# Kernel tuning notes

Measured on AMD Instinct MI355X. Metric: run time of the kernel, lower is better.

The kernel has to match this reference:

```python
import jax, jax.numpy as jnp
import numpy as np

D = 512      # d_x
H = 8        # n_I
DH = 64      # d_q = d_k = d_v = d_r
L = 4        # n_L
NUM_KNOTS = 5
ORDER = 3
KNOTS = np.linspace(-1.0, 1.0, NUM_KNOTS + ORDER)  # 8 uniform knots
EPS = 1e-5


def layernorm(x, w, b):
    mu = jnp.mean(x, axis=-1, keepdims=True)
    var = jnp.mean((x - mu) ** 2, axis=-1, keepdims=True)
    return (x - mu) * jax.lax.rsqrt(var + EPS) * w + b


def bspline_basis(x):
    # Cox-de Boor recursion on uniform knots, vectorized over all knot indices.
    # x: [...]; returns [..., len(KNOTS)-1-ORDER] = [..., 4]
    t = KNOTS
    B = jnp.stack([((t[k] <= x) & (x < t[k + 1])).astype(x.dtype)
                   for k in range(len(t) - 1)], axis=-1)
    for m in range(1, ORDER + 1):
        cols = []
        for k in range(len(t) - 1 - m):
            left = (x - t[k]) / (t[k + m] - t[k]) * B[..., k]
            right = (t[k + m + 1] - x) / (t[k + m + 1] - t[k + 1]) * B[..., k + 1]
            cols.append(left + right)
        B = jnp.stack(cols, axis=-1)
    return B


def setup_inputs() -> dict:
    key = jax.random.key(0)
    ks = jax.random.split(key, 20)
    B_, S = 4, 1024
    inp = {
        "src": jax.random.normal(ks[0], (B_, S, D), dtype=jnp.float32),
        "ln1_w": jnp.ones((L, D)), "ln1_b": jnp.zeros((L, D)),
        "ln2_w": jnp.ones((L, D)), "ln2_b": jnp.zeros((L, D)),
        "ln3_w": jnp.ones((L, D)), "ln3_b": jnp.zeros((L, D)),
        "Wq_w": jax.random.normal(ks[1], (L, H * DH, D)) * 0.02,
        "Wq_b": jnp.zeros((L, H * DH)),
        "Wk_w": jax.random.normal(ks[2], (L, H * DH, D)) * 0.02,
        "Wk_b": jnp.zeros((L, H * DH)),
        "Wv_w": jax.random.normal(ks[3], (L, H * DH, D)) * 0.02,
        "Wv_b": jnp.zeros((L, H * DH)),
        "Wr_w": jax.random.normal(ks[4], (L, H * DH, D)) * (1.0 / np.sqrt(DH)),
        "Wr_b": jnp.zeros((L, H * DH)),
        "Wo_w": jax.random.normal(ks[5], (L, D, H * DH)) * 0.02,
        "Wo_b": jnp.zeros((L, D)),
        "inner_c": jax.random.normal(ks[6], (L, D, NUM_KNOTS)) * 0.1,
        "outer_c": jax.random.normal(ks[7], (L, D, D)) * 0.1,
        "src_mask": jnp.ones((B_, 1, 1, S), dtype=jnp.int32),
    }
    return inp


def reference(src, ln1_w, ln1_b, ln2_w, ln2_b, ln3_w, ln3_b,
              Wq_w, Wq_b, Wk_w, Wk_b, Wv_w, Wv_b, Wr_w, Wr_b, Wo_w, Wo_b,
              inner_c, outer_c, src_mask):
    bsz, S, _ = src.shape
    scale = 1.0 / np.sqrt(DH)
    for l in range(L):
        # --- self-attention block ---
        z = layernorm(src, ln1_w[l], ln1_b[l])
        def heads(W, b):
            return (z @ W.T + b).reshape(bsz, S, H, DH).transpose(0, 2, 1, 3)
        Q = heads(Wq_w[l], Wq_b[l])
        K = heads(Wk_w[l], Wk_b[l])
        V = heads(Wv_w[l], Wv_b[l])
        R = heads(Wr_w[l], Wr_b[l])
        dot = jnp.einsum('bhid,bhjd->bhij', Q, K) * scale
        dot = jnp.where(src_mask == 0, -1e10, dot)
        att = jax.nn.softmax(dot, axis=-1)
        v_bar = jnp.einsum('bhjd,bhij->bhid', V, att)
        new_v = (v_bar * R).transpose(0, 2, 1, 3).reshape(bsz, S, H * DH)
        src = src + new_v @ Wo_w[l].T + Wo_b[l]
        # --- KAN feedforward block ---
        z = layernorm(src, ln2_w[l], ln2_b[l])
        xt = jnp.tanh(z)
        basis = bspline_basis(xt)            # [b,s,D,4]
        nb = NUM_KNOTS - ORDER               # only first 2 basis fns used
        inner = jnp.einsum('bsdk,dk->bsd', basis[..., :nb], inner_c[l][:, :nb])
        out = jnp.einsum('bsd,od->bso', inner, outer_c[l])
        src = src + out
        src = layernorm(src, ln3_w[l], ln3_b[l])
    return src
```

## Files before the change

### kernel.cpp

```cpp
#include <hip/hip_runtime.h>

#define B_   4
#define S_   1024
#define D_   512
#define H_   8
#define DH_  64
#define L_   4
#define NTOK (B_ * S_)
#define NT   (NTOK * D_)
#define DD   (D_ * D_)

typedef __attribute__((ext_vector_type(8))) short bf16x8;
typedef __attribute__((ext_vector_type(4))) float f32x4;

#define GLL(gp, lp)                                                            \
    __builtin_amdgcn_global_load_lds(                                          \
        (const __attribute__((address_space(1))) unsigned int*)(gp),           \
        (__attribute__((address_space(3))) unsigned int*)(lp), 16, 0, 0)

__device__ __forceinline__ float us2f(unsigned short u) {
    unsigned int v = ((unsigned int)u) << 16;
    return __uint_as_float(v);
}
__device__ __forceinline__ unsigned short f2us(float f) {
    unsigned int u = __float_as_uint(f);
    unsigned int r = (u + 0x7fffu + ((u >> 16) & 1u)) >> 16;
    return (unsigned short)r;
}
__device__ __forceinline__ unsigned short f2us_trunc(float f) {
    return (unsigned short)(__float_as_uint(f) >> 16);
}

__device__ __forceinline__ float kan_inner(float zv, const float* __restrict__ ic, int n) {
    const float kn[8] = {-1.f,
                         -0.71428571428571430f, -0.42857142857142855f, -0.14285714285714285f,
                          0.14285714285714285f,  0.42857142857142855f,  0.71428571428571430f,
                          1.f};
    float xt = tanhf(zv);
    float B0[5];
#pragma unroll
    for (int k = 0; k < 5; ++k) B0[k] = (kn[k] <= xt && xt < kn[k + 1]) ? 1.f : 0.f;
    float B1[4];
#pragma unroll
    for (int k = 0; k < 4; ++k)
        B1[k] = (xt - kn[k]) / (kn[k + 1] - kn[k]) * B0[k] +
                (kn[k + 2] - xt) / (kn[k + 2] - kn[k + 1]) * B0[k + 1];
    float B2[3];
#pragma unroll
    for (int k = 0; k < 3; ++k)
        B2[k] = (xt - kn[k]) / (kn[k + 2] - kn[k]) * B1[k] +
                (kn[k + 3] - xt) / (kn[k + 3] - kn[k + 1]) * B1[k + 1];
    float B3[2];
#pragma unroll
    for (int k = 0; k < 2; ++k)
        B3[k] = (xt - kn[k]) / (kn[k + 3] - kn[k]) * B2[k] +
                (kn[k + 4] - xt) / (kn[k + 4] - kn[k + 1]) * B2[k + 1];
    return B3[0] * ic[n * 5 + 0] + B3[1] * ic[n * 5 + 1];
}

struct PreArgs {
    const float* w[6];
    unsigned short* cw;
    const float* src;
    const float* ln1w;
    const float* ln1b;
    float* srcf;
    unsigned short* z;
};
__global__ __launch_bounds__(256) void pre_k(PreArgs a) {
    int bx = blockIdx.x;
    if (bx < 6144) {
        int y = bx >> 8;
        int l = y / 6, tp = y - l * 6;
        int i = ((bx & 255) * 256 + threadIdx.x) * 4;
        float4 v = *(const float4*)(a.w[tp] + (size_t)l * DD + i);
        ushort4 o;
        o.x = f2us(v.x); o.y = f2us(v.y); o.z = f2us(v.z); o.w = f2us(v.w);
        *(ushort4*)(a.cw + (size_t)y * DD + i) = o;
    } else {
        int wv = threadIdx.x >> 6, lane = threadIdx.x & 63;
        int tok = (bx - 6144) * 4 + wv;
        const float* xr = a.src + (size_t)tok * D_;
        float v[8];
        float s = 0.f, s2 = 0.f;
#pragma unroll
        for (int i = 0; i < 8; ++i) {
            float t = xr[lane + 64 * i];
            v[i] = t; s += t; s2 += t * t;
        }
#pragma unroll
        for (int o = 1; o < 64; o <<= 1) { s += __shfl_xor(s, o); s2 += __shfl_xor(s2, o); }
        float mu = s * (1.f / D_);
        float var = s2 * (1.f / D_) - mu * mu;
        float rs = rsqrtf(var + 1e-5f);
#pragma unroll
        for (int i = 0; i < 8; ++i) {
            int d = lane + 64 * i;
            a.srcf[(size_t)tok * D_ + d] = v[i];
            a.z[(size_t)tok * D_ + d] = f2us((v[i] - mu) * rs * a.ln1w[d] + a.ln1b[d]);
        }
    }
}

struct MGemm128Args {
    const unsigned short* A;
    const unsigned short* W[4];
    const float* bias[4];
    unsigned short* C[4];
    int tflag[4];
};

__global__ __launch_bounds__(256) void mgemm128_k(MGemm128Args g) {
    __shared__ unsigned short As[2][128 * 64];
    __shared__ unsigned short Bs[2][128 * 64];
    int z = blockIdx.z;
    const unsigned short* W = g.W[z];
    const float* bias = g.bias[z];
    unsigned short* C = g.C[z];
    int m0 = blockIdx.y * 128, n0 = blockIdx.x * 128;
    int t = threadIdx.x;
    int wave = t >> 6, lane = t & 63;
    int wm = (wave >> 1) * 64, wn = (wave & 1) * 64;
    int l15 = lane & 15, quad = lane >> 4;
    int srow = lane >> 3, schunk = lane & 7;

    f32x4 acc[4][4];
#pragma unroll
    for (int i = 0; i < 4; ++i)
#pragma unroll
        for (int j = 0; j < 4; ++j)
#pragma unroll
            for (int r = 0; r < 4; ++r) acc[i][j][r] = 0.f;

    int rb = wave * 32;
    int swz = l15 & 7;

    #define STAGE128(buf, k0)                                                       \
        do {                                                                        \
            _Pragma("unroll")                                                       \
            for (int g8 = 0; g8 < 4; ++g8) {                                        \
                int row0 = rb + g8 * 8;                                             \
                int row = row0 + srow;                                              \
                int cg = schunk ^ (row & 7);                                        \
                GLL(g.A + (size_t)(m0 + row) * D_ + (k0) + cg * 8, &As[buf][row0 * 64]); \
                GLL(W   + (size_t)(n0 + row) * D_ + (k0) + cg * 8, &Bs[buf][row0 * 64]); \
            }                                                                       \
        } while (0)

    STAGE128(0, 0);

    int cur = 0;
    for (int ks = 0; ks < 8; ++ks) {
        if (ks < 7) {
            STAGE128(cur ^ 1, (ks + 1) * 64);
            asm volatile("s_waitcnt vmcnt(8)" ::: "memory");
        } else {
            asm volatile("s_waitcnt vmcnt(0)" ::: "memory");
        }
        __builtin_amdgcn_s_barrier();
        __builtin_amdgcn_sched_barrier(0);
#pragma unroll
        for (int kc = 0; kc < 2; ++kc) {
            int ch = ((kc * 4 + quad) ^ swz) * 8;
            bf16x8 af[4], bfr[4];
#pragma unroll
            for (int mt = 0; mt < 4; ++mt)
                af[mt] = *(const bf16x8*)&As[cur][(wm + mt * 16 + l15) * 64 + ch];
#pragma unroll
            for (int nt = 0; nt < 4; ++nt)
                bfr[nt] = *(const bf16x8*)&Bs[cur][(wn + nt * 16 + l15) * 64 + ch];
#pragma unroll
            for (int mt = 0; mt < 4; ++mt)
#pragma unroll
                for (int nt = 0; nt < 4; ++nt)
                    acc[mt][nt] = __builtin_amdgcn_mfma_f32_16x16x32_bf16(
                        af[mt], bfr[nt], acc[mt][nt], 0, 0, 0);
        }
        __builtin_amdgcn_sched_barrier(0);
        __builtin_amdgcn_s_barrier();
        cur ^= 1;
    }
    #undef STAGE128

    if (g.tflag[z]) {
#pragma unroll
        for (int mt = 0; mt < 4; ++mt)
#pragma unroll
            for (int nt = 0; nt < 4; ++nt) {
                int n = n0 + wn + nt * 16 + l15;
                float bv = bias[n];
                int m = m0 + wm + mt * 16 + quad * 4;
                ushort4 pk;
                pk.x = f2us(acc[mt][nt][0] + bv);
                pk.y = f2us(acc[mt][nt][1] + bv);
                pk.z = f2us(acc[mt][nt][2] + bv);
                pk.w = f2us(acc[mt][nt][3] + bv);
                *(ushort4*)(C + ((size_t)(m >> 10) * 512 + n) * 1024 + (m & 1023)) = pk;
            }
    } else {
#pragma unroll
        for (int mt = 0; mt < 4; ++mt)
#pragma unroll
            for (int nt = 0; nt < 4; ++nt) {
                int n = n0 + wn + nt * 16 + l15;
                float bv = bias[n];
#pragma unroll
                for (int r = 0; r < 4; ++r) {
                    int m = m0 + wm + mt * 16 + quad * 4 + r;
                    C[(size_t)m * D_ + n] = f2us(acc[mt][nt][r] + bv);
                }
            }
    }
}

template <int MODE>
__global__ __launch_bounds__(512) void gemmrow_k(
    const unsigned short* __restrict__ A, const unsigned short* __restrict__ W,
    const float* __restrict__ bias, const float* __restrict__ res,
    float* __restrict__ yf, unsigned short* __restrict__ zbo,
    const float* __restrict__ wA, const float* __restrict__ bA,
    const float* __restrict__ wB, const float* __restrict__ bB,
    const float* __restrict__ ic) {
    __shared__ unsigned short Bs[2][512 * 64];
    __shared__ unsigned short As[16 * 512];
    __shared__ float redS[16][8];
    __shared__ float redS2[16][8];

    int m0 = blockIdx.x * 16;
    int t = threadIdx.x, wave = t >> 6, lane = t & 63;
    int l15 = lane & 15, quad = lane >> 4;
    int srow = lane >> 3, schunk = lane & 7;
    int swz = l15 & 7;

#pragma unroll
    for (int rr = 0; rr < 2; ++rr) {
        int r = wave * 2 + rr;
        GLL(A + (size_t)(m0 + r) * D_ + (lane ^ (r & 7)) * 8, &As[r * 512]);
    }
    const unsigned short* Wp = W + (size_t)(wave * 64 + srow) * D_ + (schunk ^ srow) * 8;
#pragma unroll
    for (int g8 = 0; g8 < 8; ++g8)
        GLL(Wp + (size_t)g8 * 8 * D_, &Bs[0][(wave * 64 + g8 * 8) * 64]);
    asm volatile("s_waitcnt vmcnt(8)" ::: "memory");
    __builtin_amdgcn_s_barrier();

    f32x4 acc[4];
#pragma unroll
    for (int nt = 0; nt < 4; ++nt)
#pragma unroll
        for (int r = 0; r < 4; ++r) acc[nt][r] = 0.f;

    int cur = 0;
    for (int ks = 0; ks < 8; ++ks) {
        __builtin_amdgcn_sched_barrier(0);
        if (ks < 7) {
#pragma unroll
            for (int g8 = 0; g8 < 8; ++g8)
                GLL(Wp + (ks + 1) * 64 + (size_t)g8 * 8 * D_,
                    &Bs[cur ^ 1][(wave * 64 + g8 * 8) * 64]);
            asm volatile("s_waitcnt vmcnt(8)" ::: "memory");
        } else {
            asm volatile("s_waitcnt vmcnt(0)" ::: "memory");
        }
        __builtin_amdgcn_sched_barrier(0);
#pragma unroll
        for (int kc = 0; kc < 2; ++kc) {
            bf16x8 af = *(const bf16x8*)&As[l15 * 512 + ((ks * 8 + kc * 4 + quad) ^ swz) * 8];
#pragma unroll
            for (int nt = 0; nt < 4; ++nt) {
                bf16x8 bf = *(const bf16x8*)&Bs[cur][(wave * 64 + nt * 16 + l15) * 64 +
                                                     ((kc * 4 + quad) ^ swz) * 8];
                acc[nt] = __builtin_amdgcn_mfma_f32_16x16x32_bf16(af, bf, acc[nt], 0, 0, 0);
            }
        }
        cur ^= 1;
    }

    float tv[4][4];
#pragma unroll
    for (int nt = 0; nt < 4; ++nt) {
        int n = wave * 64 + nt * 16 + l15;
        float bv = (MODE == 0) ? bias[n] : 0.f;
#pragma unroll
        for (int r = 0; r < 4; ++r)
            tv[nt][r] = acc[nt][r] + bv + res[(size_t)(m0 + quad * 4 + r) * D_ + n];
    }
    if (MODE == 0) {
#pragma unroll
        for (int nt = 0; nt < 4; ++nt) {
            int n = wave * 64 + nt * 16 + l15;
#pragma unroll
            for (int r = 0; r < 4; ++r)
                yf[(size_t)(m0 + quad * 4 + r) * D_ + n] = tv[nt][r];
        }
    }

    float s[4] = {0.f, 0.f, 0.f, 0.f}, s2[4] = {0.f, 0.f, 0.f, 0.f};
#pragma unroll
    for (int nt = 0; nt < 4; ++nt)
#pragma unroll
        for (int r = 0; r < 4; ++r) { s[r] += tv[nt][r]; s2[r] += tv[nt][r] * tv[nt][r]; }
#pragma unroll
    for (int off = 1; off < 16; off <<= 1)
#pragma unroll
        for (int r = 0; r < 4; ++r) { s[r] += __shfl_xor(s[r], off); s2[r] += __shfl_xor(s2[r], off); }
    if (l15 == 0) {
#pragma unroll
        for (int r = 0; r < 4; ++r) { redS[quad * 4 + r][wave] = s[r]; redS2[quad * 4 + r][wave] = s2[r]; }
    }
    __syncthreads();
    float mu[4], rs[4];
#pragma unroll
    for (int r = 0; r < 4; ++r) {
        float ss = 0.f, ss2 = 0.f;
#pragma unroll
        for (int w = 0; w < 8; ++w) { ss += redS[quad * 4 + r][w]; ss2 += redS2[quad * 4 + r][w]; }
        mu[r] = ss * (1.f / D_);
        float var = ss2 * (1.f / D_) - mu[r] * mu[r];
        rs[r] = rsqrtf(var + 1e-5f);
    }

    if (MODE == 0) {
#pragma unroll
        for (int nt = 0; nt < 4; ++nt) {
            int n = wave * 64 + nt * 16 + l15;
#pragma unroll
            for (int r = 0; r < 4; ++r) {
                float zv = (tv[nt][r] - mu[r]) * rs[r] * wA[n] + bA[n];
                zbo[(size_t)(m0 + quad * 4 + r) * D_ + n] = f2us(kan_inner(zv, ic, n));
            }
        }
    } else {
        float yv[4][4];
#pragma unroll
        for (int nt = 0; nt < 4; ++nt) {
            int n = wave * 64 + nt * 16 + l15;
#pragma unroll
            for (int r = 0; r < 4; ++r) {
                float v = (tv[nt][r] - mu[r]) * rs[r] * wA[n] + bA[n];
                yv[nt][r] = v;
                yf[(size_t)(m0 + quad * 4 + r) * D_ + n] = v;
            }
        }
        if (MODE == 1) {
            __syncthreads();
            float sb[4] = {0.f, 0.f, 0.f, 0.f}, sb2[4] = {0.f, 0.f, 0.f, 0.f};
#pragma unroll
            for (int nt = 0; nt < 4; ++nt)
#pragma unroll
                for (int r = 0; r < 4; ++r) { sb[r] += yv[nt][r]; sb2[r] += yv[nt][r] * yv[nt][r]; }
#pragma unroll
            for (int off = 1; off < 16; off <<= 1)
#pragma unroll
                for (int r = 0; r < 4; ++r) { sb[r] += __shfl_xor(sb[r], off); sb2[r] += __shfl_xor(sb2[r], off); }
            if (l15 == 0) {
#pragma unroll
                for (int r = 0; r < 4; ++r) { redS[quad * 4 + r][wave] = sb[r]; redS2[quad * 4 + r][wave] = sb2[r]; }
            }
            __syncthreads();
#pragma unroll
            for (int r = 0; r < 4; ++r) {
                float ss = 0.f, ss2 = 0.f;
#pragma unroll
                for (int w = 0; w < 8; ++w) { ss += redS[quad * 4 + r][w]; ss2 += redS2[quad * 4 + r][w]; }
                float mu1 = ss * (1.f / D_);
                float var1 = ss2 * (1.f / D_) - mu1 * mu1;
                float rs1 = rsqrtf(var1 + 1e-5f);
#pragma unroll
                for (int nt = 0; nt < 4; ++nt) {
                    int n = wave * 64 + nt * 16 + l15;
                    zbo[(size_t)(m0 + quad * 4 + r) * D_ + n] =
                        f2us((yv[nt][r] - mu1) * rs1 * wB[n] + bB[n]);
                }
            }
        }
    }
}

__global__ __launch_bounds__(256) void attn_k(const unsigned short* __restrict__ Q,
                                              const unsigned short* __restrict__ K,
                                              const unsigned short* __restrict__ vt,
                                              const unsigned short* __restrict__ R,
                                              const int* __restrict__ mask,
                                              unsigned short* __restrict__ O) {
    __shared__ unsigned short Ks[2][64 * 64];
    __shared__ unsigned short Vts[2][64 * 64];
    __shared__ unsigned short Ps[4][16][72];
    __shared__ float Ms[1024];

    int bh = blockIdx.x;
    int b = bh >> 3, h = bh & 7;
    int qt0 = blockIdx.y * 64;
    int t = threadIdx.x, wave = t >> 6, lane = t & 63;
    int l15 = lane & 15, quad = lane >> 4;
    int qw0 = qt0 + wave * 16;

    const unsigned short* Qrow = Q + ((size_t)(b * S_ + qw0 + l15) * H_ + h) * DH_;
    bf16x8 qf[2];
    qf[0] = *(const bf16x8*)(Qrow + quad * 8);
    qf[1] = *(const bf16x8*)(Qrow + 32 + quad * 8);

#pragma unroll
    for (int u = 0; u < 4; ++u)
        Ms[u * 256 + t] = mask[b * S_ + u * 256 + t] ? 0.f : -1e10f;
    asm volatile("s_waitcnt lgkmcnt(0)" ::: "memory");

    float lsum[4] = {0.f, 0.f, 0.f, 0.f};
    f32x4 acc_o[4];
#pragma unroll
    for (int dt = 0; dt < 4; ++dt)
#pragma unroll
        for (int r = 0; r < 4; ++r) acc_o[dt][r] = 0.f;

    int lro = lane >> 3;
    int cglob = (lane & 7) ^ lro;
    const unsigned short* kgp0 =
        K + ((size_t)(b * S_ + wave * 16 + lro) * H_ + h) * DH_ + cglob * 8;
    const unsigned short* vgp0 =
        vt + (size_t)(b * 512 + h * 64 + wave * 16 + lro) * 1024 + cglob * 8;
    int swz = l15 & 7;
    const float SC = 0.125f * 1.44269504089f;

    #define ASTAGE(buf, kt)                                                         \
        do {                                                                        \
            GLL(kgp0 + (size_t)(kt) * 64 * 512,           &Ks[buf][(wave * 16) * 64]);     \
            GLL(kgp0 + (size_t)(kt) * 64 * 512 + 8 * 512, &Ks[buf][(wave * 16 + 8) * 64]); \
            GLL(vgp0 + (kt) * 64,                         &Vts[buf][(wave * 16) * 64]);    \
            GLL(vgp0 + (kt) * 64 + 8 * 1024,              &Vts[buf][(wave * 16 + 8) * 64]);\
        } while (0)

    ASTAGE(0, 0);

    int cur = 0;
    for (int kt = 0; kt < 16; ++kt) {
        if (kt < 15) {
            ASTAGE(cur ^ 1, kt + 1);
            asm volatile("s_waitcnt vmcnt(4)" ::: "memory");
        } else {
            asm volatile("s_waitcnt vmcnt(0)" ::: "memory");
        }
        __builtin_amdgcn_s_barrier();
        __builtin_amdgcn_sched_barrier(0);

        f32x4 accs[4];
#pragma unroll
        for (int jt = 0; jt < 4; ++jt)
#pragma unroll
            for (int r = 0; r < 4; ++r) accs[jt][r] = 0.f;
        __builtin_amdgcn_s_setprio(1);
#pragma unroll
        for (int kc = 0; kc < 2; ++kc) {
            int ch = ((kc * 4 + quad) ^ swz) * 8;
#pragma unroll
            for (int jt = 0; jt < 4; ++jt) {
                bf16x8 kf = *(const bf16x8*)&Ks[cur][(jt * 16 + l15) * 64 + ch];
                accs[jt] = __builtin_amdgcn_mfma_f32_16x16x32_bf16(qf[kc], kf, accs[jt], 0, 0, 0);
            }
        }
        __builtin_amdgcn_s_setprio(0);

#pragma unroll
        for (int jt = 0; jt < 4; ++jt) {
            float madd = Ms[kt * 64 + jt * 16 + l15];
#pragma unroll
            for (int r = 0; r < 4; ++r) {
                float p = __builtin_amdgcn_exp2f(accs[jt][r] * SC + madd);
                lsum[r] += p;
                Ps[wave][quad * 4 + r][jt * 16 + l15] = f2us_trunc(p);
            }
        }

        __builtin_amdgcn_s_setprio(1);
#pragma unroll
        for (int kc = 0; kc < 2; ++kc) {
            bf16x8 pf = *(const bf16x8*)&Ps[wave][l15][kc * 32 + quad * 8];
            int ch = ((kc * 4 + quad) ^ swz) * 8;
#pragma unroll
            for (int dt = 0; dt < 4; ++dt) {
                bf16x8 vf = *(const bf16x8*)&Vts[cur][(dt * 16 + l15) * 64 + ch];
                acc_o[dt] = __builtin_amdgcn_mfma_f32_16x16x32_bf16(pf, vf, acc_o[dt], 0, 0, 0);
            }
        }
        __builtin_amdgcn_s_setprio(0);

        __builtin_amdgcn_sched_barrier(0);
        __builtin_amdgcn_s_barrier();
        cur ^= 1;
    }
    #undef ASTAGE

#pragma unroll
    for (int off = 1; off < 16; off <<= 1)
#pragma unroll
        for (int r = 0; r < 4; ++r) lsum[r] += __shfl_xor(lsum[r], off);

#pragma unroll
    for (int r = 0; r < 4; ++r) {
        int q = qw0 + quad * 4 + r;
        float inv = 1.f / lsum[r];
        const unsigned short* Rr = R + ((size_t)(b * S_ + q) * H_ + h) * DH_;
        unsigned short* Or = O + ((size_t)(b * S_ + q) * H_ + h) * DH_;
#pragma unroll
        for (int dt = 0; dt < 4; ++dt) {
            int d = dt * 16 + l15;
            Or[d] = f2us(acc_o[dt][r] * inv * us2f(Rr[d]));
        }
    }
}

extern "C" void kernel_launch(void* const* d_in, const int* in_sizes, int n_in,
                              void* d_out, int out_size, void* d_ws, size_t ws_size,
                              hipStream_t stream) {
    const float* src  = (const float*)d_in[0];
    const float* ln1w = (const float*)d_in[1];
    const float* ln1b = (const float*)d_in[2];
    const float* ln2w = (const float*)d_in[3];
    const float* ln2b = (const float*)d_in[4];
    const float* ln3w = (const float*)d_in[5];
    const float* ln3b = (const float*)d_in[6];
    const float* wq   = (const float*)d_in[7];
    const float* wqb  = (const float*)d_in[8];
    const float* wk   = (const float*)d_in[9];
    const float* wkb  = (const float*)d_in[10];
    const float* wv   = (const float*)d_in[11];
    const float* wvb  = (const float*)d_in[12];
    const float* wr   = (const float*)d_in[13];
    const float* wrb  = (const float*)d_in[14];
    const float* wo   = (const float*)d_in[15];
    const float* wob  = (const float*)d_in[16];
    const float* ic   = (const float*)d_in[17];
    const float* oc   = (const float*)d_in[18];
    const int* mask   = (const int*)d_in[19];
    float* out = (float*)d_out;

    float* srcf = (float*)d_ws;
    unsigned short* zb = (unsigned short*)(srcf + NT);
    unsigned short* qb = zb + NT;
    unsigned short* kb = qb + NT;
    unsigned short* vb = kb + NT;
    unsigned short* rb = vb + NT;
    unsigned short* cw = rb + NT;

    PreArgs pa;
    pa.w[0] = wq; pa.w[1] = wk; pa.w[2] = wv;
    pa.w[3] = wr; pa.w[4] = wo; pa.w[5] = oc;
    pa.cw = cw; pa.src = src; pa.ln1w = ln1w; pa.ln1b = ln1b;
    pa.srcf = srcf; pa.z = zb;
    pre_k<<<dim3(6144 + NTOK / 4), dim3(256), 0, stream>>>(pa);

    for (int l = 0; l < L_; ++l) {
        unsigned short* cwl = cw + (size_t)l * 6 * DD;

        MGemm128Args ga;
        ga.A = zb;
        ga.W[0] = cwl + 0 * DD; ga.bias[0] = wqb + l * D_; ga.C[0] = qb; ga.tflag[0] = 0;
        ga.W[1] = cwl + 1 * DD; ga.bias[1] = wkb + l * D_; ga.C[1] = kb; ga.tflag[1] = 0;
        ga.W[2] = cwl + 2 * DD; ga.bias[2] = wvb + l * D_; ga.C[2] = vb; ga.tflag[2] = 1;
        ga.W[3] = cwl + 3 * DD; ga.bias[3] = wrb + l * D_; ga.C[3] = rb; ga.tflag[3] = 0;
        mgemm128_k<<<dim3(4, 32, 4), dim3(256), 0, stream>>>(ga);

        attn_k<<<dim3(32, 16), dim3(256), 0, stream>>>(qb, kb, vb, rb, mask, zb);

        gemmrow_k<0><<<dim3(NTOK / 16), dim3(512), 0, stream>>>(
            zb, cwl + 4 * DD, wob + l * D_, srcf, srcf, zb,
            ln2w + l * D_, ln2b + l * D_, nullptr, nullptr, ic + (size_t)l * D_ * 5);

        if (l < L_ - 1)
            gemmrow_k<1><<<dim3(NTOK / 16), dim3(512), 0, stream>>>(
                zb, cwl + 5 * DD, nullptr, srcf, srcf, zb,
                ln3w + l * D_, ln3b + l * D_, ln1w + (l + 1) * D_, ln1b + (l + 1) * D_,
                nullptr);
        else
            gemmrow_k<2><<<dim3(NTOK / 16), dim3(512), 0, stream>>>(
                zb, cwl + 5 * DD, nullptr, srcf, out, nullptr,
                ln3w + l * D_, ln3b + l * D_, nullptr, nullptr, nullptr);
    }
}
```

Baseline: 421.7 us.

## Transpose QK^T MFMA output for packed P stores; swizzle multi-GEMM block order

The attention kernel swaps the MFMA operands so each lane holds four consecutive key scores for one query. That lets P be written to LDS as a single 8-byte packed store per tile, with a perm instruction doing the bf16 conversion. It also lets the row sum be kept in one scalar per lane and reduced with two shuffles instead of sixteen. Separately, the fused QKVR GEMM remaps its block indices so that consecutively launched blocks are spread across the z/m/n tiles, intended to improve cache locality or balance across XCDs.

```diff
diff --git a/kernel.cpp b/kernel.cpp
--- a/kernel.cpp
+++ b/kernel.cpp
@@ -26,9 +26,6 @@
     unsigned int u = __float_as_uint(f);
     unsigned int r = (u + 0x7fffu + ((u >> 16) & 1u)) >> 16;
     return (unsigned short)r;
-}
-__device__ __forceinline__ unsigned short f2us_trunc(float f) {
-    return (unsigned short)(__float_as_uint(f) >> 16);
 }
 
 __device__ __forceinline__ float kan_inner(float zv, const float* __restrict__ ic, int n) {
@@ -113,11 +110,13 @@
 __global__ __launch_bounds__(256) void mgemm128_k(MGemm128Args g) {
     __shared__ unsigned short As[2][128 * 64];
     __shared__ unsigned short Bs[2][128 * 64];
-    int z = blockIdx.z;
+    int id = blockIdx.x + (blockIdx.y << 2) + (blockIdx.z << 7);
+    int id2 = ((id & 7) << 6) + (id >> 3);
+    int z = id2 >> 7;
     const unsigned short* W = g.W[z];
     const float* bias = g.bias[z];
     unsigned short* C = g.C[z];
-    int m0 = blockIdx.y * 128, n0 = blockIdx.x * 128;
+    int m0 = ((id2 >> 2) & 31) * 128, n0 = (id2 & 3) * 128;
     int t = threadIdx.x;
     int wave = t >> 6, lane = t & 63;
     int wm = (wave >> 1) * 64, wn = (wave & 1) * 64;
@@ -405,7 +404,7 @@
         Ms[u * 256 + t] = mask[b * S_ + u * 256 + t] ? 0.f : -1e10f;
     asm volatile("s_waitcnt lgkmcnt(0)" ::: "memory");
 
-    float lsum[4] = {0.f, 0.f, 0.f, 0.f};
+    float lsum = 0.f;
     f32x4 acc_o[4];
 #pragma unroll
     for (int dt = 0; dt < 4; ++dt)
@@ -454,20 +453,23 @@
 #pragma unroll
             for (int jt = 0; jt < 4; ++jt) {
                 bf16x8 kf = *(const bf16x8*)&Ks[cur][(jt * 16 + l15) * 64 + ch];
-                accs[jt] = __builtin_amdgcn_mfma_f32_16x16x32_bf16(qf[kc], kf, accs[jt], 0, 0, 0);
+                accs[jt] = __builtin_amdgcn_mfma_f32_16x16x32_bf16(kf, qf[kc], accs[jt], 0, 0, 0);
             }
         }
         __builtin_amdgcn_s_setprio(0);
 
 #pragma unroll
         for (int jt = 0; jt < 4; ++jt) {
-            float madd = Ms[kt * 64 + jt * 16 + l15];
-#pragma unroll
-            for (int r = 0; r < 4; ++r) {
-                float p = __builtin_amdgcn_exp2f(accs[jt][r] * SC + madd);
-                lsum[r] += p;
-                Ps[wave][quad * 4 + r][jt * 16 + l15] = f2us_trunc(p);
-            }
+            int kb = kt * 64 + jt * 16 + quad * 4;
+            float p0 = __builtin_amdgcn_exp2f(accs[jt][0] * SC + Ms[kb + 0]);
+            float p1 = __builtin_amdgcn_exp2f(accs[jt][1] * SC + Ms[kb + 1]);
+            float p2 = __builtin_amdgcn_exp2f(accs[jt][2] * SC + Ms[kb + 2]);
+            float p3 = __builtin_amdgcn_exp2f(accs[jt][3] * SC + Ms[kb + 3]);
+            lsum += (p0 + p1) + (p2 + p3);
+            uint2 pk;
+            pk.x = __builtin_amdgcn_perm(__float_as_uint(p1), __float_as_uint(p0), 0x07060302u);
+            pk.y = __builtin_amdgcn_perm(__float_as_uint(p3), __float_as_uint(p2), 0x07060302u);
+            *(uint2*)&Ps[wave][l15][jt * 16 + quad * 4] = pk;
         }
 
         __builtin_amdgcn_s_setprio(1);
@@ -489,15 +491,14 @@
     }
     #undef ASTAGE
 
-#pragma unroll
-    for (int off = 1; off < 16; off <<= 1)
-#pragma unroll
-        for (int r = 0; r < 4; ++r) lsum[r] += __shfl_xor(lsum[r], off);
+    lsum += __shfl_xor(lsum, 16);
+    lsum += __shfl_xor(lsum, 32);
 
 #pragma unroll
     for (int r = 0; r < 4; ++r) {
-        int q = qw0 + quad * 4 + r;
-        float inv = 1.f / lsum[r];
+        int qq = quad * 4 + r;
+        int q = qw0 + qq;
+        float inv = 1.f / __shfl(lsum, qq);
         const unsigned short* Rr = R + ((size_t)(b * S_ + q) * H_ + h) * DH_;
         unsigned short* Or = O + ((size_t)(b * S_ + q) * H_ + h) * DH_;
 #pragma unroll
```

After: 421.2 us. Within noise of the previous version (-0.1%).
